# Optimization experiments

Hardware: AMD Instinct MI355X
Metric: run time of the kernel (lower is better)

## Reference

```python
import jax, jax.numpy as jnp
import numpy as np

L, H, D, E, V, MAXS = 12, 12, 64, 768, 50257, 1024

def _ln(x, g, b, eps=1e-5):
    m = jnp.mean(x, axis=-1, keepdims=True)
    v = jnp.mean(jnp.square(x - m), axis=-1, keepdims=True)
    return (x - m) * jax.lax.rsqrt(v + eps) * g + b

def setup_inputs() -> dict:
    key = jax.random.key(0)
    ks = jax.random.split(key, 16)
    s = 0.02
    inp = {
        "input_ids": jax.random.randint(ks[0], (1, 1), 0, V),
        "past_key": jax.random.normal(ks[1], (L, 1, H, MAXS, D), jnp.float32),
        "past_value": jax.random.normal(ks[2], (L, 1, H, MAXS, D), jnp.float32),
        "past_seq_len": 1023,
        "attention_mask": jnp.ones((1, MAXS), jnp.float32),
        "wte": jax.random.normal(ks[3], (V, E), jnp.float32) * s,
        "wpe": jax.random.normal(ks[4], (MAXS, E), jnp.float32) * s,
        "ln1_g": jnp.ones((L, E), jnp.float32),
        "ln1_b": jnp.zeros((L, E), jnp.float32),
        "attn_w": jax.random.normal(ks[5], (L, E, 3 * E), jnp.float32) * s,
        "attn_b": jnp.zeros((L, 3 * E), jnp.float32),
        "proj_w": jax.random.normal(ks[6], (L, E, E), jnp.float32) * s,
        "proj_b": jnp.zeros((L, E), jnp.float32),
        "ln2_g": jnp.ones((L, E), jnp.float32),
        "ln2_b": jnp.zeros((L, E), jnp.float32),
        "fc_w": jax.random.normal(ks[7], (L, E, 4 * E), jnp.float32) * s,
        "fc_b": jnp.zeros((L, 4 * E), jnp.float32),
        "mlp_w": jax.random.normal(ks[8], (L, 4 * E, E), jnp.float32) * s,
        "mlp_b": jnp.zeros((L, E), jnp.float32),
        "lnf_g": jnp.ones((E,), jnp.float32),
        "lnf_b": jnp.zeros((E,), jnp.float32),
    }
    return inp

def reference(input_ids, past_key, past_value, past_seq_len, attention_mask,
              wte, wpe, ln1_g, ln1_b, attn_w, attn_b, proj_w, proj_b,
              ln2_g, ln2_b, fc_w, fc_b, mlp_w, mlp_b, lnf_g, lnf_b):
    S = int(past_seq_len)  # static cache length
    h = wte[input_ids] + wpe[S]                      # [1,1,E]
    bias = (1.0 - attention_mask[:, :S + 1]) * -1e9  # [1,S+1]
    scale = 1.0 / jnp.sqrt(jnp.float32(D))
    pk, pv = past_key, past_value
    for l in range(L):
        x = _ln(h, ln1_g[l], ln1_b[l])
        qkv = x @ attn_w[l] + attn_b[l]              # [1,1,3E]
        q, k, v = jnp.split(qkv, 3, axis=-1)
        q = q.reshape(1, 1, H, D).transpose(0, 2, 1, 3)  # [1,H,1,D]
        k = k.reshape(1, 1, H, D).transpose(0, 2, 1, 3)
        v = v.reshape(1, 1, H, D).transpose(0, 2, 1, 3)
        k_full = jnp.concatenate([pk[l, :, :, :S, :], k], axis=2)  # [1,H,S+1,D]
        v_full = jnp.concatenate([pv[l, :, :, :S, :], v], axis=2)
        scores = jnp.einsum('bhqd,bhkd->bhqk', q, k_full) * scale
        scores = scores + bias[:, None, None, :]
        attn = jax.nn.softmax(scores, axis=-1)
        o = jnp.einsum('bhqk,bhkd->bhqd', attn, v_full)
        o = o.transpose(0, 2, 1, 3).reshape(1, 1, H * D)
        h = h + o @ proj_w[l] + proj_b[l]
        x2 = _ln(h, ln2_g[l], ln2_b[l])
        h = h + jax.nn.gelu(x2 @ fc_w[l] + fc_b[l], approximate=True) @ mlp_w[l] + mlp_b[l]
        pk = pk.at[l, :, :, S, :].set(k[:, :, 0, :])
        pv = pv.at[l, :, :, S, :].set(v[:, :, 0, :])
    h = _ln(h, lnf_g, lnf_b)
    logits = h @ wte.T                               # [1,1,V] (tied lm_head)
    return (logits, pk, pv)
```

## Files before the change

### kernel.cpp

```cpp
#include <hip/hip_runtime.h>
#include <math.h>

#define EMB 768
#define NH 12
#define HD 64
#define NL 12
#define NV 50257
#define MAXS 1024
#define S_PAST 1023
#define E3 2304
#define E4 3072

#define WS_H    0
#define WS_QKV  768
#define WS_FC   3072
#define WS_PART 6144

__device__ __forceinline__ void blockReduce2(float& a, float& b, volatile float* ra, volatile float* rb) {
  int lane = threadIdx.x & 63, wid = threadIdx.x >> 6;
#pragma unroll
  for (int o = 32; o > 0; o >>= 1) { a += __shfl_down(a, o); b += __shfl_down(b, o); }
  if (lane == 0) { ra[wid] = a; rb[wid] = b; }
  __syncthreads();
  if (threadIdx.x == 0) {
    ra[0] = ra[0] + ra[1] + ra[2] + ra[3];
    rb[0] = rb[0] + rb[1] + rb[2] + rb[3];
  }
  __syncthreads();
  a = ra[0]; b = rb[0];
}

__global__ void init_kernel(const int* __restrict__ ids, const float* __restrict__ wte,
                            const float* __restrict__ wpe, const float* __restrict__ attn_b,
                            float* __restrict__ hvec, float* __restrict__ qkv) {
  int idx = blockIdx.x * 256 + threadIdx.x;
  if (idx < E3) qkv[idx] = attn_b[idx];
  if (idx < EMB) {
    int id = ids[0];
    hvec[idx] = wte[(size_t)id * EMB + idx] + wpe[(size_t)S_PAST * EMB + idx];
  }
}

__global__ void ln_gemv4(const float* __restrict__ hvec, const float* __restrict__ g,
                         const float* __restrict__ bb, const float* __restrict__ W,
                         float* __restrict__ out, int N, int l) {
  __shared__ float lh[EMB];
  __shared__ float xs[32];
  __shared__ float ra[4], rb[4];
  __shared__ float4 red[4][64];
  int tid = threadIdx.x, lane = tid & 63, wid = tid >> 6;
  int e0 = blockIdx.y * 32;
  float hv0 = hvec[tid], hv1 = hvec[tid + 256], hv2 = hvec[tid + 512];
  int j4 = blockIdx.x * 64 + lane;
  int N4 = N >> 2;
  const float4* p = (const float4*)(W + (size_t)l * EMB * N) + (size_t)(e0 + wid) * N4 + j4;
  float4 w[8];
#pragma unroll
  for (int i = 0; i < 8; i++) w[i] = p[(size_t)(i * 4) * N4];
  float gv = 0.f, bv = 0.f;
  if (tid < 32) { gv = g[l * EMB + e0 + tid]; bv = bb[l * EMB + e0 + tid]; }
  lh[tid] = hv0; lh[tid + 256] = hv1; lh[tid + 512] = hv2;
  float s1 = hv0 + hv1 + hv2;
  float s2 = hv0 * hv0 + hv1 * hv1 + hv2 * hv2;
  blockReduce2(s1, s2, ra, rb);
  float mean = s1 * (1.f / EMB);
  float var = s2 * (1.f / EMB) - mean * mean;
  float rstd = rsqrtf(var + 1e-5f);
  if (tid < 32) xs[tid] = (lh[e0 + tid] - mean) * rstd * gv + bv;
  __syncthreads();
  float4 acc = {0.f, 0.f, 0.f, 0.f};
#pragma unroll
  for (int i = 0; i < 8; i++) {
    float x = xs[wid + i * 4];
    acc.x += x * w[i].x; acc.y += x * w[i].y; acc.z += x * w[i].z; acc.w += x * w[i].w;
  }
  red[wid][lane] = acc;
  __syncthreads();
  if (wid == 0) {
    float4 a0 = red[0][lane], a1 = red[1][lane], a2 = red[2][lane], a3 = red[3][lane];
    float rx = a0.x + a1.x + a2.x + a3.x;
    float ry = a0.y + a1.y + a2.y + a3.y;
    float rz = a0.z + a1.z + a2.z + a3.z;
    float rw = a0.w + a1.w + a2.w + a3.w;
    float* op = out + (size_t)j4 * 4;
    atomicAdd(op + 0, rx); atomicAdd(op + 1, ry);
    atomicAdd(op + 2, rz); atomicAdd(op + 3, rw);
  }
}

__global__ void attn_kv(const float* __restrict__ qkv, const float* __restrict__ pk,
                        const float* __restrict__ pv, const float* __restrict__ mask,
                        float* __restrict__ opk, float* __restrict__ opv,
                        float* __restrict__ part, int l) {
  int h = blockIdx.x >> 4, c = blockIdx.x & 15;
  int tid = threadIdx.x, lane = tid & 63, wid = tid >> 6;
  int sub = tid & 15, grp = tid >> 4;
  __shared__ float4 qs4[16];
  __shared__ float sc[64];
  __shared__ float4 redo[4][16];
  if (tid < 16) qs4[tid] = ((const float4*)(qkv + h * 64))[tid];
  __syncthreads();
  size_t base = ((size_t)(l * NH + h) * MAXS) * HD;
  const float4* K4 = (const float4*)(pk + base);
  const float4* V4 = (const float4*)(pv + base);
  float4* oK4 = (float4*)(opk + base);
  float4* oV4 = (float4*)(opv + base);
  int t0 = c * 64;
  float4 kreg[4];
#pragma unroll
  for (int i = 0; i < 4; i++) {
    int t = t0 + grp + i * 16;
    kreg[i] = (t == S_PAST) ? ((const float4*)(qkv + EMB + h * 64))[sub] : K4[(size_t)t * 16 + sub];
  }
#pragma unroll
  for (int i = 0; i < 4; i++) {
    int t = t0 + grp + i * 16;
    oK4[(size_t)t * 16 + sub] = kreg[i];
  }
  float4 q4 = qs4[sub];
#pragma unroll
  for (int i = 0; i < 4; i++) {
    int key = grp + i * 16;
    float p = q4.x * kreg[i].x + q4.y * kreg[i].y + q4.z * kreg[i].z + q4.w * kreg[i].w;
    p += __shfl_xor(p, 1); p += __shfl_xor(p, 2);
    p += __shfl_xor(p, 4); p += __shfl_xor(p, 8);
    if (sub == 0) sc[key] = p * 0.125f + (1.f - mask[t0 + key]) * (-1e9f);
  }
  __syncthreads();
  if (wid == 0) {
    float a = sc[lane];
    float m = a;
#pragma unroll
    for (int o = 32; o > 0; o >>= 1) m = fmaxf(m, __shfl_down(m, o));
    m = __shfl(m, 0);
    float ea = expf(a - m);
    sc[lane] = ea;
    float s = ea;
#pragma unroll
    for (int o = 32; o > 0; o >>= 1) s += __shfl_down(s, o);
    if (lane == 0) { part[(h * 16 + c) * 68 + 0] = m; part[(h * 16 + c) * 68 + 1] = s; }
  }
  __syncthreads();
  float4 vreg[4];
#pragma unroll
  for (int i = 0; i < 4; i++) {
    int t = t0 + grp + i * 16;
    vreg[i] = (t == S_PAST) ? ((const float4*)(qkv + 2 * EMB + h * 64))[sub] : V4[(size_t)t * 16 + sub];
  }
#pragma unroll
  for (int i = 0; i < 4; i++) {
    int t = t0 + grp + i * 16;
    oV4[(size_t)t * 16 + sub] = vreg[i];
  }
  float4 acc = {0.f, 0.f, 0.f, 0.f};
#pragma unroll
  for (int i = 0; i < 4; i++) {
    float w = sc[grp + i * 16];
    acc.x += w * vreg[i].x; acc.y += w * vreg[i].y; acc.z += w * vreg[i].z; acc.w += w * vreg[i].w;
  }
  acc.x += __shfl_xor(acc.x, 16); acc.y += __shfl_xor(acc.y, 16);
  acc.z += __shfl_xor(acc.z, 16); acc.w += __shfl_xor(acc.w, 16);
  acc.x += __shfl_xor(acc.x, 32); acc.y += __shfl_xor(acc.y, 32);
  acc.z += __shfl_xor(acc.z, 32); acc.w += __shfl_xor(acc.w, 32);
  if (lane < 16) redo[wid][lane] = acc;
  __syncthreads();
  if (tid < 16) {
    float4 a0 = redo[0][tid], a1 = redo[1][tid], a2 = redo[2][tid], a3 = redo[3][tid];
    float4 r;
    r.x = a0.x + a1.x + a2.x + a3.x;
    r.y = a0.y + a1.y + a2.y + a3.y;
    r.z = a0.z + a1.z + a2.z + a3.z;
    r.w = a0.w + a1.w + a2.w + a3.w;
    ((float4*)(part + (h * 16 + c) * 68 + 4))[tid] = r;
  }
}

__global__ void proj_attn(const float* __restrict__ part, const float* __restrict__ W,
                          const float* __restrict__ bias, const float* __restrict__ fc_b,
                          float* __restrict__ hout, float* __restrict__ wfc, int l) {
  int jb = blockIdx.x;
  int rt = blockIdx.y;
  int h = rt >> 2, esub = rt & 3;
  int tid = threadIdx.x, lane = tid & 63, wid = tid >> 6;
  __shared__ float xs[16];
  __shared__ float4 red[4][64];
  int j4 = jb * 64 + lane;
  const int N4 = EMB >> 2;
  int r0 = h * 64 + esub * 16;
  const float4* p = (const float4*)(W + (size_t)l * EMB * EMB) + (size_t)(r0 + wid) * N4 + j4;
  float4 w[4];
#pragma unroll
  for (int i = 0; i < 4; i++) w[i] = p[(size_t)(i * 4) * N4];
  if (tid < 16) {
    float M = -1e30f;
#pragma unroll
    for (int q = 0; q < 16; q++) M = fmaxf(M, part[(h * 16 + q) * 68]);
    float T = 0.f, o = 0.f;
    int d = esub * 16 + tid;
#pragma unroll
    for (int q = 0; q < 16; q++) {
      float wq = expf(part[(h * 16 + q) * 68] - M);
      T += part[(h * 16 + q) * 68 + 1] * wq;
      o += part[(h * 16 + q) * 68 + 4 + d] * wq;
    }
    xs[tid] = o / T;
  }
  int bid = rt * 3 + jb;
  if (bid < 12) wfc[bid * 256 + tid] = fc_b[l * E4 + bid * 256 + tid];
  __syncthreads();
  float4 acc = {0.f, 0.f, 0.f, 0.f};
#pragma unroll
  for (int i = 0; i < 4; i++) {
    float x = xs[wid + i * 4];
    acc.x += x * w[i].x; acc.y += x * w[i].y; acc.z += x * w[i].z; acc.w += x * w[i].w;
  }
  red[wid][lane] = acc;
  __syncthreads();
  if (wid == 0) {
    float4 a0 = red[0][lane], a1 = red[1][lane], a2 = red[2][lane], a3 = red[3][lane];
    float rx = a0.x + a1.x + a2.x + a3.x;
    float ry = a0.y + a1.y + a2.y + a3.y;
    float rz = a0.z + a1.z + a2.z + a3.z;
    float rw = a0.w + a1.w + a2.w + a3.w;
    if (rt == 0) {
      const float* bp = bias + l * EMB + jb * 256 + lane * 4;
      rx += bp[0]; ry += bp[1]; rz += bp[2]; rw += bp[3];
    }
    float* op = hout + (size_t)jb * 256 + (size_t)lane * 4;
    atomicAdd(op + 0, rx); atomicAdd(op + 1, ry);
    atomicAdd(op + 2, rz); atomicAdd(op + 3, rw);
  }
}

__global__ void mlp_gemv4(const float* __restrict__ fcv, const float* __restrict__ W,
                          const float* __restrict__ bias, const float* __restrict__ attn_b,
                          float* __restrict__ hout, float* __restrict__ qkv, int l) {
  __shared__ float xs[64];
  __shared__ float4 red[4][64];
  int tid = threadIdx.x, lane = tid & 63, wid = tid >> 6;
  int e0 = blockIdx.y * 64;
  int j4 = blockIdx.x * 64 + lane;
  const int N4 = EMB >> 2;
  const float4* p = (const float4*)(W + (size_t)l * E4 * EMB) + (size_t)(e0 + wid) * N4 + j4;
  float4 w[16];
#pragma unroll
  for (int i = 0; i < 16; i++) w[i] = p[(size_t)(i * 4) * N4];
  if (tid < 64) {
    float x = fcv[e0 + tid];
    xs[tid] = 0.5f * x * (1.f + tanhf(0.7978845608028654f * (x + 0.044715f * x * x * x)));
  }
  int bid = blockIdx.y * 3 + blockIdx.x;
  if (l + 1 < NL && bid < 9) qkv[bid * 256 + tid] = attn_b[(l + 1) * E3 + bid * 256 + tid];
  __syncthreads();
  float4 acc = {0.f, 0.f, 0.f, 0.f};
#pragma unroll
  for (int i = 0; i < 16; i++) {
    float x = xs[wid + i * 4];
    acc.x += x * w[i].x; acc.y += x * w[i].y; acc.z += x * w[i].z; acc.w += x * w[i].w;
  }
  red[wid][lane] = acc;
  __syncthreads();
  if (wid == 0) {
    float4 a0 = red[0][lane], a1 = red[1][lane], a2 = red[2][lane], a3 = red[3][lane];
    float rx = a0.x + a1.x + a2.x + a3.x;
    float ry = a0.y + a1.y + a2.y + a3.y;
    float rz = a0.z + a1.z + a2.z + a3.z;
    float rw = a0.w + a1.w + a2.w + a3.w;
    if (blockIdx.y == 0) {
      const float* bp = bias + l * EMB + j4 * 4;
      rx += bp[0]; ry += bp[1]; rz += bp[2]; rw += bp[3];
    }
    float* op = hout + (size_t)j4 * 4;
    atomicAdd(op + 0, rx); atomicAdd(op + 1, ry);
    atomicAdd(op + 2, rz); atomicAdd(op + 3, rw);
  }
}

__global__ void logits_lnf(const float* __restrict__ hvec, const float* __restrict__ g,
                           const float* __restrict__ b, const float* __restrict__ wte,
                           float* __restrict__ out) {
  __shared__ float4 xs4[192];
  __shared__ float ra[4], rb[4];
  int tid = threadIdx.x, lane = tid & 63, wid = tid >> 6;
  float hv0 = hvec[tid], hv1 = hvec[tid + 256], hv2 = hvec[tid + 512];
  int v = blockIdx.x * 4 + wid;
  float4 a0 = {0,0,0,0}, a1 = {0,0,0,0}, a2 = {0,0,0,0};
  if (v < NV) {
    const float4* row = (const float4*)(wte + (size_t)v * EMB);
    a0 = row[lane]; a1 = row[lane + 64]; a2 = row[lane + 128];
  }
  float s1 = hv0 + hv1 + hv2;
  float s2 = hv0 * hv0 + hv1 * hv1 + hv2 * hv2;
  blockReduce2(s1, s2, ra, rb);
  float mean = s1 * (1.f / EMB);
  float var = s2 * (1.f / EMB) - mean * mean;
  float rstd = rsqrtf(var + 1e-5f);
  ((float*)xs4)[tid]       = (hv0 - mean) * rstd * g[tid]       + b[tid];
  ((float*)xs4)[tid + 256] = (hv1 - mean) * rstd * g[tid + 256] + b[tid + 256];
  ((float*)xs4)[tid + 512] = (hv2 - mean) * rstd * g[tid + 512] + b[tid + 512];
  __syncthreads();
  if (v >= NV) return;
  float4 x0 = xs4[lane], x1 = xs4[lane + 64], x2 = xs4[lane + 128];
  float acc = a0.x * x0.x + a0.y * x0.y + a0.z * x0.z + a0.w * x0.w
            + a1.x * x1.x + a1.y * x1.y + a1.z * x1.z + a1.w * x1.w
            + a2.x * x2.x + a2.y * x2.y + a2.z * x2.z + a2.w * x2.w;
#pragma unroll
  for (int o = 32; o > 0; o >>= 1) acc += __shfl_down(acc, o);
  if (lane == 0) out[v] = acc;
}

extern "C" void kernel_launch(void* const* d_in, const int* in_sizes, int n_in,
                              void* d_out, int out_size, void* d_ws, size_t ws_size,
                              hipStream_t stream) {
  const int* input_ids = (const int*)d_in[0];
  const float* past_key = (const float*)d_in[1];
  const float* past_value = (const float*)d_in[2];
  const float* mask = (const float*)d_in[4];
  const float* wte = (const float*)d_in[5];
  const float* wpe = (const float*)d_in[6];
  const float* ln1_g = (const float*)d_in[7];
  const float* ln1_b = (const float*)d_in[8];
  const float* attn_w = (const float*)d_in[9];
  const float* attn_b = (const float*)d_in[10];
  const float* proj_w = (const float*)d_in[11];
  const float* proj_b = (const float*)d_in[12];
  const float* ln2_g = (const float*)d_in[13];
  const float* ln2_b = (const float*)d_in[14];
  const float* fc_w = (const float*)d_in[15];
  const float* fc_b = (const float*)d_in[16];
  const float* mlp_w = (const float*)d_in[17];
  const float* mlp_b = (const float*)d_in[18];
  const float* lnf_g = (const float*)d_in[19];
  const float* lnf_b = (const float*)d_in[20];

  float* out = (float*)d_out;
  float* out_logits = out;
  float* out_pk = out + NV;
  float* out_pv = out_pk + (size_t)NL * NH * MAXS * HD;

  float* ws = (float*)d_ws;
  float* wh = ws + WS_H;
  float* wqkv = ws + WS_QKV;
  float* wfc = ws + WS_FC;
  float* wpart = ws + WS_PART;

  init_kernel<<<9, 256, 0, stream>>>(input_ids, wte, wpe, attn_b, wh, wqkv);

  for (int l = 0; l < NL; l++) {
    ln_gemv4<<<dim3(9, 24), 256, 0, stream>>>(wh, ln1_g, ln1_b, attn_w, wqkv, E3, l);
    attn_kv<<<192, 256, 0, stream>>>(wqkv, past_key, past_value, mask, out_pk, out_pv, wpart, l);
    proj_attn<<<dim3(3, 48), 256, 0, stream>>>(wpart, proj_w, proj_b, fc_b, wh, wfc, l);
    ln_gemv4<<<dim3(12, 24), 256, 0, stream>>>(wh, ln2_g, ln2_b, fc_w, wfc, E4, l);
    mlp_gemv4<<<dim3(3, 48), 256, 0, stream>>>(wfc, mlp_w, mlp_b, attn_b, wh, wqkv, l);
  }
  logits_lnf<<<12565, 256, 0, stream>>>(wh, lnf_g, lnf_b, wte, out_logits);
}
```

Baseline: 448.5 us.

## Fuse LN1 and QKV projection into attention kernel, handle new token separately

```diff
diff --git a/kernel.cpp b/kernel.cpp
--- a/kernel.cpp
+++ b/kernel.cpp
@@ -12,9 +12,17 @@
 #define E4 3072
 
 #define WS_H    0
-#define WS_QKV  768
-#define WS_FC   3072
-#define WS_PART 6144
+#define WS_FC   768
+#define WS_PART 3840
+#define WS_VNEW 16896
+#define WS_DOT  17088
+
+__device__ __forceinline__ void f4add(float4& a, const float4& b) {
+  a.x += b.x; a.y += b.y; a.z += b.z; a.w += b.w;
+}
+__device__ __forceinline__ void f4fma(float4& a, float x, const float4& w) {
+  a.x += x * w.x; a.y += x * w.y; a.z += x * w.z; a.w += x * w.w;
+}
 
 __device__ __forceinline__ void blockReduce2(float& a, float& b, volatile float* ra, volatile float* rb) {
   int lane = threadIdx.x & 63, wid = threadIdx.x >> 6;
@@ -30,103 +38,152 @@
   a = ra[0]; b = rb[0];
 }
 
+__device__ __forceinline__ float gelu(float x) {
+  return 0.5f * x * (1.f + tanhf(0.7978845608028654f * (x + 0.044715f * x * x * x)));
+}
+
 __global__ void init_kernel(const int* __restrict__ ids, const float* __restrict__ wte,
-                            const float* __restrict__ wpe, const float* __restrict__ attn_b,
-                            float* __restrict__ hvec, float* __restrict__ qkv) {
-  int idx = blockIdx.x * 256 + threadIdx.x;
-  if (idx < E3) qkv[idx] = attn_b[idx];
-  if (idx < EMB) {
-    int id = ids[0];
-    hvec[idx] = wte[(size_t)id * EMB + idx] + wpe[(size_t)S_PAST * EMB + idx];
-  }
-}
-
-__global__ void ln_gemv4(const float* __restrict__ hvec, const float* __restrict__ g,
-                         const float* __restrict__ bb, const float* __restrict__ W,
-                         float* __restrict__ out, int N, int l) {
-  __shared__ float lh[EMB];
-  __shared__ float xs[32];
-  __shared__ float ra[4], rb[4];
-  __shared__ float4 red[4][64];
+                            const float* __restrict__ wpe, float* __restrict__ wsf) {
+  int tid = threadIdx.x;
+  int id = ids[0];
+#pragma unroll
+  for (int k = 0; k < 3; k++) {
+    int e = tid + 256 * k;
+    wsf[WS_H + e] = wte[(size_t)id * EMB + e] + wpe[(size_t)S_PAST * EMB + e];
+  }
+  if (tid < NL * NH) wsf[WS_DOT + tid] = 0.f;
+}
+
+__global__ void attn_fused(const float* __restrict__ pk, const float* __restrict__ pv,
+                           const float* __restrict__ mask,
+                           const float* __restrict__ ln1_g, const float* __restrict__ ln1_b,
+                           const float* __restrict__ attn_w, const float* __restrict__ attn_b,
+                           float* __restrict__ opk, float* __restrict__ opv,
+                           float* __restrict__ wsf, int l) {
+  __shared__ __align__(16) float smem[1936];
+  float* xs = smem;
+  volatile float* ra = smem + 768;
+  volatile float* rb = smem + 772;
+  float4* qls = (float4*)(smem + 776);
+  float* sc = smem + 848;
+  float4* red = (float4*)(smem + 912);
+  int bi = blockIdx.x;
+  int h = bi % NH, c = bi / NH;
   int tid = threadIdx.x, lane = tid & 63, wid = tid >> 6;
-  int e0 = blockIdx.y * 32;
-  float hv0 = hvec[tid], hv1 = hvec[tid + 256], hv2 = hvec[tid + 512];
-  int j4 = blockIdx.x * 64 + lane;
-  int N4 = N >> 2;
-  const float4* p = (const float4*)(W + (size_t)l * EMB * N) + (size_t)(e0 + wid) * N4 + j4;
-  float4 w[8];
-#pragma unroll
-  for (int i = 0; i < 8; i++) w[i] = p[(size_t)(i * 4) * N4];
-  float gv = 0.f, bv = 0.f;
-  if (tid < 32) { gv = g[l * EMB + e0 + tid]; bv = bb[l * EMB + e0 + tid]; }
-  lh[tid] = hv0; lh[tid + 256] = hv1; lh[tid + 512] = hv2;
-  float s1 = hv0 + hv1 + hv2;
-  float s2 = hv0 * hv0 + hv1 * hv1 + hv2 * hv2;
+  int sub = tid & 15, grp = tid >> 4;
+  const float* wh = wsf + WS_H;
+  float hv0 = wh[tid], hv1 = wh[tid + 256], hv2 = wh[tid + 512];
+  size_t base = ((size_t)(l * NH + h) * MAXS) * HD;
+  const float4* K4 = (const float4*)(pk + base);
+  const float4* V4 = (const float4*)(pv + base);
+  int t0 = c * 64;
+  float4 kreg[4];
+#pragma unroll
+  for (int i = 0; i < 4; i++) {
+    int t = t0 + grp + i * 16;
+    kreg[i] = K4[(size_t)t * 16 + sub];
+  }
+  float gv0 = ln1_g[l * EMB + tid], gv1 = ln1_g[l * EMB + tid + 256], gv2 = ln1_g[l * EMB + tid + 512];
+  float bv0 = ln1_b[l * EMB + tid], bv1 = ln1_b[l * EMB + tid + 256], bv2 = ln1_b[l * EMB + tid + 512];
+  float s1 = hv0 + hv1 + hv2, s2 = hv0 * hv0 + hv1 * hv1 + hv2 * hv2;
   blockReduce2(s1, s2, ra, rb);
   float mean = s1 * (1.f / EMB);
   float var = s2 * (1.f / EMB) - mean * mean;
   float rstd = rsqrtf(var + 1e-5f);
-  if (tid < 32) xs[tid] = (lh[e0 + tid] - mean) * rstd * gv + bv;
-  __syncthreads();
-  float4 acc = {0.f, 0.f, 0.f, 0.f};
-#pragma unroll
-  for (int i = 0; i < 8; i++) {
-    float x = xs[wid + i * 4];
-    acc.x += x * w[i].x; acc.y += x * w[i].y; acc.z += x * w[i].z; acc.w += x * w[i].w;
-  }
-  red[wid][lane] = acc;
-  __syncthreads();
-  if (wid == 0) {
-    float4 a0 = red[0][lane], a1 = red[1][lane], a2 = red[2][lane], a3 = red[3][lane];
-    float rx = a0.x + a1.x + a2.x + a3.x;
-    float ry = a0.y + a1.y + a2.y + a3.y;
-    float rz = a0.z + a1.z + a2.z + a3.z;
-    float rw = a0.w + a1.w + a2.w + a3.w;
-    float* op = out + (size_t)j4 * 4;
-    atomicAdd(op + 0, rx); atomicAdd(op + 1, ry);
-    atomicAdd(op + 2, rz); atomicAdd(op + 3, rw);
-  }
-}
-
-__global__ void attn_kv(const float* __restrict__ qkv, const float* __restrict__ pk,
-                        const float* __restrict__ pv, const float* __restrict__ mask,
-                        float* __restrict__ opk, float* __restrict__ opv,
-                        float* __restrict__ part, int l) {
-  int h = blockIdx.x >> 4, c = blockIdx.x & 15;
-  int tid = threadIdx.x, lane = tid & 63, wid = tid >> 6;
-  int sub = tid & 15, grp = tid >> 4;
-  __shared__ float4 qs4[16];
-  __shared__ float sc[64];
-  __shared__ float4 redo[4][16];
-  if (tid < 16) qs4[tid] = ((const float4*)(qkv + h * 64))[tid];
-  __syncthreads();
-  size_t base = ((size_t)(l * NH + h) * MAXS) * HD;
-  const float4* K4 = (const float4*)(pk + base);
-  const float4* V4 = (const float4*)(pv + base);
-  float4* oK4 = (float4*)(opk + base);
-  float4* oV4 = (float4*)(opv + base);
-  int t0 = c * 64;
-  float4 kreg[4];
-#pragma unroll
-  for (int i = 0; i < 4; i++) {
-    int t = t0 + grp + i * 16;
-    kreg[i] = (t == S_PAST) ? ((const float4*)(qkv + EMB + h * 64))[sub] : K4[(size_t)t * 16 + sub];
-  }
-#pragma unroll
-  for (int i = 0; i < 4; i++) {
-    int t = t0 + grp + i * 16;
-    oK4[(size_t)t * 16 + sub] = kreg[i];
-  }
-  float4 q4 = qs4[sub];
+  xs[tid]       = (hv0 - mean) * rstd * gv0 + bv0;
+  xs[tid + 256] = (hv1 - mean) * rstd * gv1 + bv1;
+  xs[tid + 512] = (hv2 - mean) * rstd * gv2 + bv2;
+  __syncthreads();
+  const float4* Wb4 = (const float4*)(attn_w + (size_t)l * EMB * E3);
+  const int STR = E3 >> 2;
+  const float4* Wq4 = Wb4 + h * 16 + sub;
+  float4 qacc = {0.f, 0.f, 0.f, 0.f};
+#pragma unroll
+  for (int b = 0; b < 4; b++) {
+    float4 w[12];
+#pragma unroll
+    for (int j = 0; j < 12; j++) w[j] = Wq4[(size_t)(grp + 16 * (b * 12 + j)) * STR];
+#pragma unroll
+    for (int j = 0; j < 12; j++) f4fma(qacc, xs[grp + 16 * (b * 12 + j)], w[j]);
+  }
+  red[tid] = qacc;
+  __syncthreads();
+#pragma unroll
+  for (int s = 8; s >= 1; s >>= 1) {
+    if (tid < s * 16) f4add(red[tid], red[tid + s * 16]);
+    __syncthreads();
+  }
+  if (tid < 16) {
+    float4 q = red[tid];
+    f4add(q, ((const float4*)(attn_b + l * E3 + h * 64))[tid]);
+    qls[tid] = q;
+  }
+  __syncthreads();
+  const float4* Wk4 = Wb4 + 192 + h * 16 + c;
+  const float4* Wv4 = Wb4 + 384 + h * 16 + c;
+  float4 ak = {0.f, 0.f, 0.f, 0.f}, av = {0.f, 0.f, 0.f, 0.f};
+  {
+    float4 wk[3], wv[3];
+#pragma unroll
+    for (int j = 0; j < 3; j++) {
+      int r = tid + 256 * j;
+      wk[j] = Wk4[(size_t)r * STR]; wv[j] = Wv4[(size_t)r * STR];
+    }
+#pragma unroll
+    for (int j = 0; j < 3; j++) {
+      int r = tid + 256 * j;
+      f4fma(ak, xs[r], wk[j]); f4fma(av, xs[r], wv[j]);
+    }
+  }
+  red[tid] = ak;
+  __syncthreads();
+#pragma unroll
+  for (int s = 128; s >= 1; s >>= 1) {
+    if (tid < s) f4add(red[tid], red[tid + s]);
+    __syncthreads();
+  }
+  if (tid == 0) {
+    float4 kn = red[0];
+    f4add(kn, ((const float4*)(attn_b + l * E3))[192 + h * 16 + c]);
+    qls[16] = kn;
+  }
+  __syncthreads();
+  red[tid] = av;
+  __syncthreads();
+#pragma unroll
+  for (int s = 128; s >= 1; s >>= 1) {
+    if (tid < s) f4add(red[tid], red[tid + s]);
+    __syncthreads();
+  }
+  if (tid == 0) {
+    float4 vn = red[0];
+    f4add(vn, ((const float4*)(attn_b + l * E3))[384 + h * 16 + c]);
+    float4 kn = qls[16];
+    const float* qf = (const float*)qls;
+    float d4 = qf[c * 4] * kn.x + qf[c * 4 + 1] * kn.y + qf[c * 4 + 2] * kn.z + qf[c * 4 + 3] * kn.w;
+    atomicAdd(wsf + WS_DOT + l * NH + h, d4);
+    ((float4*)(opk + base))[(size_t)S_PAST * 16 + c] = kn;
+    ((float4*)(opv + base))[(size_t)S_PAST * 16 + c] = vn;
+    ((float4*)(wsf + WS_VNEW))[h * 16 + c] = vn;
+  }
+  float4 q4 = qls[sub];
 #pragma unroll
   for (int i = 0; i < 4; i++) {
     int key = grp + i * 16;
+    int t = t0 + key;
     float p = q4.x * kreg[i].x + q4.y * kreg[i].y + q4.z * kreg[i].z + q4.w * kreg[i].w;
     p += __shfl_xor(p, 1); p += __shfl_xor(p, 2);
     p += __shfl_xor(p, 4); p += __shfl_xor(p, 8);
-    if (sub == 0) sc[key] = p * 0.125f + (1.f - mask[t0 + key]) * (-1e9f);
-  }
-  __syncthreads();
+    if (sub == 0) sc[key] = (t == S_PAST) ? -1e9f : p * 0.125f + (1.f - mask[t]) * (-1e9f);
+  }
+  float4 vreg[4];
+#pragma unroll
+  for (int i = 0; i < 4; i++) {
+    int t = t0 + grp + i * 16;
+    vreg[i] = V4[(size_t)t * 16 + sub];
+  }
+  __syncthreads();
+  float* part = wsf + WS_PART;
   if (wid == 0) {
     float a = sc[lane];
     float m = a;
@@ -141,31 +198,20 @@
     if (lane == 0) { part[(h * 16 + c) * 68 + 0] = m; part[(h * 16 + c) * 68 + 1] = s; }
   }
   __syncthreads();
-  float4 vreg[4];
-#pragma unroll
-  for (int i = 0; i < 4; i++) {
-    int t = t0 + grp + i * 16;
-    vreg[i] = (t == S_PAST) ? ((const float4*)(qkv + 2 * EMB + h * 64))[sub] : V4[(size_t)t * 16 + sub];
-  }
-#pragma unroll
-  for (int i = 0; i < 4; i++) {
-    int t = t0 + grp + i * 16;
-    oV4[(size_t)t * 16 + sub] = vreg[i];
-  }
   float4 acc = {0.f, 0.f, 0.f, 0.f};
 #pragma unroll
   for (int i = 0; i < 4; i++) {
     float w = sc[grp + i * 16];
-    acc.x += w * vreg[i].x; acc.y += w * vreg[i].y; acc.z += w * vreg[i].z; acc.w += w * vreg[i].w;
+    f4fma(acc, w, vreg[i]);
   }
   acc.x += __shfl_xor(acc.x, 16); acc.y += __shfl_xor(acc.y, 16);
   acc.z += __shfl_xor(acc.z, 16); acc.w += __shfl_xor(acc.w, 16);
   acc.x += __shfl_xor(acc.x, 32); acc.y += __shfl_xor(acc.y, 32);
   acc.z += __shfl_xor(acc.z, 32); acc.w += __shfl_xor(acc.w, 32);
-  if (lane < 16) redo[wid][lane] = acc;
+  if (lane < 16) red[wid * 16 + lane] = acc;
   __syncthreads();
   if (tid < 16) {
-    float4 a0 = redo[0][tid], a1 = redo[1][tid], a2 = redo[2][tid], a3 = redo[3][tid];
+    float4 a0 = red[tid], a1 = red[16 + tid], a2 = red[32 + tid], a3 = red[48 + tid];
     float4 r;
     r.x = a0.x + a1.x + a2.x + a3.x;
     r.y = a0.y + a1.y + a2.y + a3.y;
@@ -173,17 +219,27 @@
     r.w = a0.w + a1.w + a2.w + a3.w;
     ((float4*)(part + (h * 16 + c) * 68 + 4))[tid] = r;
   }
-}
-
-__global__ void proj_attn(const float* __restrict__ part, const float* __restrict__ W,
-                          const float* __restrict__ bias, const float* __restrict__ fc_b,
-                          float* __restrict__ hout, float* __restrict__ wfc, int l) {
+#pragma unroll
+  for (int i = 0; i < 4; i++) {
+    int t = t0 + grp + i * 16;
+    if (t != S_PAST) {
+      ((float4*)(opk + base))[(size_t)t * 16 + sub] = kreg[i];
+      ((float4*)(opv + base))[(size_t)t * 16 + sub] = vreg[i];
+    }
+  }
+}
+
+__global__ void proj_attn(const float* __restrict__ W, const float* __restrict__ bias,
+                          const float* __restrict__ fc_b, const float* __restrict__ mask,
+                          float* __restrict__ hout, float* __restrict__ wsf, int l) {
   int jb = blockIdx.x;
   int rt = blockIdx.y;
   int h = rt >> 2, esub = rt & 3;
   int tid = threadIdx.x, lane = tid & 63, wid = tid >> 6;
   __shared__ float xs[16];
   __shared__ float4 red[4][64];
+  const float* part = wsf + WS_PART;
+  float* wfc = wsf + WS_FC;
   int j4 = jb * 64 + lane;
   const int N4 = EMB >> 2;
   int r0 = h * 64 + esub * 16;
@@ -192,11 +248,13 @@
 #pragma unroll
   for (int i = 0; i < 4; i++) w[i] = p[(size_t)(i * 4) * N4];
   if (tid < 16) {
-    float M = -1e30f;
+    float dot8 = wsf[WS_DOT + l * NH + h] * 0.125f + (1.f - mask[S_PAST]) * (-1e9f);
+    float M = dot8;
 #pragma unroll
     for (int q = 0; q < 16; q++) M = fmaxf(M, part[(h * 16 + q) * 68]);
-    float T = 0.f, o = 0.f;
+    float en = expf(dot8 - M);
     int d = esub * 16 + tid;
+    float T = en, o = en * wsf[WS_VNEW + h * 64 + d];
 #pragma unroll
     for (int q = 0; q < 16; q++) {
       float wq = expf(part[(h * 16 + q) * 68] - M);
@@ -210,10 +268,7 @@
   __syncthreads();
   float4 acc = {0.f, 0.f, 0.f, 0.f};
 #pragma unroll
-  for (int i = 0; i < 4; i++) {
-    float x = xs[wid + i * 4];
-    acc.x += x * w[i].x; acc.y += x * w[i].y; acc.z += x * w[i].z; acc.w += x * w[i].w;
-  }
+  for (int i = 0; i < 4; i++) f4fma(acc, xs[wid + i * 4], w[i]);
   red[wid][lane] = acc;
   __syncthreads();
   if (wid == 0) {
@@ -232,9 +287,52 @@
   }
 }
 
+__global__ void fc_gemv(const float* __restrict__ hvec, const float* __restrict__ g,
+                        const float* __restrict__ bb, const float* __restrict__ W,
+                        float* __restrict__ wfc, int l) {
+  __shared__ float lh[EMB];
+  __shared__ float xs[48];
+  __shared__ float ra[4], rb[4];
+  __shared__ float4 red[4][64];
+  int tid = threadIdx.x, lane = tid & 63, wid = tid >> 6;
+  int jt = blockIdx.x, et = blockIdx.y;
+  int e0 = et * 48;
+  float hv0 = hvec[tid], hv1 = hvec[tid + 256], hv2 = hvec[tid + 512];
+  int j4 = jt * 64 + lane;
+  const int N4 = E4 >> 2;
+  const float4* p = (const float4*)(W + (size_t)l * EMB * E4) + (size_t)(e0 + wid) * N4 + j4;
+  float4 w[12];
+#pragma unroll
+  for (int i = 0; i < 12; i++) w[i] = p[(size_t)(i * 4) * N4];
+  float gv = 0.f, bv = 0.f;
+  if (tid < 48) { gv = g[l * EMB + e0 + tid]; bv = bb[l * EMB + e0 + tid]; }
+  lh[tid] = hv0; lh[tid + 256] = hv1; lh[tid + 512] = hv2;
+  float s1 = hv0 + hv1 + hv2, s2 = hv0 * hv0 + hv1 * hv1 + hv2 * hv2;
+  blockReduce2(s1, s2, ra, rb);
+  float mean = s1 * (1.f / EMB);
+  float var = s2 * (1.f / EMB) - mean * mean;
+  float rstd = rsqrtf(var + 1e-5f);
+  if (tid < 48) xs[tid] = (lh[e0 + tid] - mean) * rstd * gv + bv;
+  __syncthreads();
+  float4 acc = {0.f, 0.f, 0.f, 0.f};
+#pragma unroll
+  for (int i = 0; i < 12; i++) f4fma(acc, xs[wid + i * 4], w[i]);
+  red[wid][lane] = acc;
+  __syncthreads();
+  if (wid == 0) {
+    float4 a0 = red[0][lane], a1 = red[1][lane], a2 = red[2][lane], a3 = red[3][lane];
+    float rx = a0.x + a1.x + a2.x + a3.x;
+    float ry = a0.y + a1.y + a2.y + a3.y;
+    float rz = a0.z + a1.z + a2.z + a3.z;
+    float rw = a0.w + a1.w + a2.w + a3.w;
+    float* op = wfc + (size_t)j4 * 4;
+    atomicAdd(op + 0, rx); atomicAdd(op + 1, ry);
+    atomicAdd(op + 2, rz); atomicAdd(op + 3, rw);
+  }
+}
+
 __global__ void mlp_gemv4(const float* __restrict__ fcv, const float* __restrict__ W,
-                          const float* __restrict__ bias, const float* __restrict__ attn_b,
-                          float* __restrict__ hout, float* __restrict__ qkv, int l) {
+                          const float* __restrict__ bias, float* __restrict__ hout, int l) {
   __shared__ float xs[64];
   __shared__ float4 red[4][64];
   int tid = threadIdx.x, lane = tid & 63, wid = tid >> 6;
@@ -245,19 +343,11 @@
   float4 w[16];
 #pragma unroll
   for (int i = 0; i < 16; i++) w[i] = p[(size_t)(i * 4) * N4];
-  if (tid < 64) {
-    float x = fcv[e0 + tid];
-    xs[tid] = 0.5f * x * (1.f + tanhf(0.7978845608028654f * (x + 0.044715f * x * x * x)));
-  }
-  int bid = blockIdx.y * 3 + blockIdx.x;
-  if (l + 1 < NL && bid < 9) qkv[bid * 256 + tid] = attn_b[(l + 1) * E3 + bid * 256 + tid];
+  if (tid < 64) xs[tid] = gelu(fcv[e0 + tid]);
   __syncthreads();
   float4 acc = {0.f, 0.f, 0.f, 0.f};
 #pragma unroll
-  for (int i = 0; i < 16; i++) {
-    float x = xs[wid + i * 4];
-    acc.x += x * w[i].x; acc.y += x * w[i].y; acc.z += x * w[i].z; acc.w += x * w[i].w;
-  }
+  for (int i = 0; i < 16; i++) f4fma(acc, xs[wid + i * 4], w[i]);
   red[wid][lane] = acc;
   __syncthreads();
   if (wid == 0) {
@@ -279,7 +369,7 @@
 __global__ void logits_lnf(const float* __restrict__ hvec, const float* __restrict__ g,
                            const float* __restrict__ b, const float* __restrict__ wte,
                            float* __restrict__ out) {
-  __shared__ float4 xs4[192];
+  __shared__ __align__(16) float4 xs4[192];
   __shared__ float ra[4], rb[4];
   int tid = threadIdx.x, lane = tid & 63, wid = tid >> 6;
   float hv0 = hvec[tid], hv1 = hvec[tid + 256], hv2 = hvec[tid + 512];
@@ -337,21 +427,18 @@
   float* out_logits = out;
   float* out_pk = out + NV;
   float* out_pv = out_pk + (size_t)NL * NH * MAXS * HD;
-
-  float* ws = (float*)d_ws;
-  float* wh = ws + WS_H;
-  float* wqkv = ws + WS_QKV;
-  float* wfc = ws + WS_FC;
-  float* wpart = ws + WS_PART;
-
-  init_kernel<<<9, 256, 0, stream>>>(input_ids, wte, wpe, attn_b, wh, wqkv);
+  float* wsf = (float*)d_ws;
+  float* wh = wsf + WS_H;
+  float* wfc = wsf + WS_FC;
+
+  init_kernel<<<1, 256, 0, stream>>>(input_ids, wte, wpe, wsf);
 
   for (int l = 0; l < NL; l++) {
-    ln_gemv4<<<dim3(9, 24), 256, 0, stream>>>(wh, ln1_g, ln1_b, attn_w, wqkv, E3, l);
-    attn_kv<<<192, 256, 0, stream>>>(wqkv, past_key, past_value, mask, out_pk, out_pv, wpart, l);
-    proj_attn<<<dim3(3, 48), 256, 0, stream>>>(wpart, proj_w, proj_b, fc_b, wh, wfc, l);
-    ln_gemv4<<<dim3(12, 24), 256, 0, stream>>>(wh, ln2_g, ln2_b, fc_w, wfc, E4, l);
-    mlp_gemv4<<<dim3(3, 48), 256, 0, stream>>>(wfc, mlp_w, mlp_b, attn_b, wh, wqkv, l);
+    attn_fused<<<192, 256, 0, stream>>>(past_key, past_value, mask, ln1_g, ln1_b,
+                                        attn_w, attn_b, out_pk, out_pv, wsf, l);
+    proj_attn<<<dim3(3, 48), 256, 0, stream>>>(proj_w, proj_b, fc_b, mask, wh, wsf, l);
+    fc_gemv<<<dim3(12, 16), 256, 0, stream>>>(wh, ln2_g, ln2_b, fc_w, wfc, l);
+    mlp_gemv4<<<dim3(3, 48), 256, 0, stream>>>(wfc, mlp_w, mlp_b, wh, l);
   }
   logits_lnf<<<12565, 256, 0, stream>>>(wh, lnf_g, lnf_b, wte, out_logits);
 }
```

Result: slower. 500.5 us (+11.6%).

## Fuse FC and MLP GEMVs into one kernel with double-buffered hidden state

Applied to the files above, without the earlier changes.

```diff
diff --git a/kernel.cpp b/kernel.cpp
--- a/kernel.cpp
+++ b/kernel.cpp
@@ -11,10 +11,17 @@
 #define E3 2304
 #define E4 3072
 
-#define WS_H    0
-#define WS_QKV  768
-#define WS_FC   3072
-#define WS_PART 6144
+#define WS_HA   0
+#define WS_HB   768
+#define WS_QKV  1536
+#define WS_PART 3840
+
+__device__ __forceinline__ void f4add(float4& a, const float4& b) {
+  a.x += b.x; a.y += b.y; a.z += b.z; a.w += b.w;
+}
+__device__ __forceinline__ void f4fma(float4& a, float x, const float4& w) {
+  a.x += x * w.x; a.y += x * w.y; a.z += x * w.z; a.w += x * w.w;
+}
 
 __device__ __forceinline__ void blockReduce2(float& a, float& b, volatile float* ra, volatile float* rb) {
   int lane = threadIdx.x & 63, wid = threadIdx.x >> 6;
@@ -30,20 +37,24 @@
   a = ra[0]; b = rb[0];
 }
 
+__device__ __forceinline__ float gelu(float x) {
+  return 0.5f * x * (1.f + tanhf(0.7978845608028654f * (x + 0.044715f * x * x * x)));
+}
+
 __global__ void init_kernel(const int* __restrict__ ids, const float* __restrict__ wte,
                             const float* __restrict__ wpe, const float* __restrict__ attn_b,
-                            float* __restrict__ hvec, float* __restrict__ qkv) {
+                            float* __restrict__ wsf) {
   int idx = blockIdx.x * 256 + threadIdx.x;
-  if (idx < E3) qkv[idx] = attn_b[idx];
+  if (idx < E3) wsf[WS_QKV + idx] = attn_b[idx];
   if (idx < EMB) {
     int id = ids[0];
-    hvec[idx] = wte[(size_t)id * EMB + idx] + wpe[(size_t)S_PAST * EMB + idx];
-  }
-}
-
-__global__ void ln_gemv4(const float* __restrict__ hvec, const float* __restrict__ g,
-                         const float* __restrict__ bb, const float* __restrict__ W,
-                         float* __restrict__ out, int N, int l) {
+    wsf[WS_HA + idx] = wte[(size_t)id * EMB + idx] + wpe[(size_t)S_PAST * EMB + idx];
+  }
+}
+
+__global__ void ln_gemv4(const float* __restrict__ hvec, float* __restrict__ shadow,
+                         const float* __restrict__ g, const float* __restrict__ bb,
+                         const float* __restrict__ W, float* __restrict__ out, int l) {
   __shared__ float lh[EMB];
   __shared__ float xs[32];
   __shared__ float ra[4], rb[4];
@@ -52,13 +63,16 @@
   int e0 = blockIdx.y * 32;
   float hv0 = hvec[tid], hv1 = hvec[tid + 256], hv2 = hvec[tid + 512];
   int j4 = blockIdx.x * 64 + lane;
-  int N4 = N >> 2;
-  const float4* p = (const float4*)(W + (size_t)l * EMB * N) + (size_t)(e0 + wid) * N4 + j4;
+  const int N4 = E3 >> 2;
+  const float4* p = (const float4*)(W + (size_t)l * EMB * E3) + (size_t)(e0 + wid) * N4 + j4;
   float4 w[8];
 #pragma unroll
   for (int i = 0; i < 8; i++) w[i] = p[(size_t)(i * 4) * N4];
   float gv = 0.f, bv = 0.f;
   if (tid < 32) { gv = g[l * EMB + e0 + tid]; bv = bb[l * EMB + e0 + tid]; }
+  if (blockIdx.x == 0 && blockIdx.y == 0) {
+    shadow[tid] = hv0; shadow[tid + 256] = hv1; shadow[tid + 512] = hv2;
+  }
   lh[tid] = hv0; lh[tid + 256] = hv1; lh[tid + 512] = hv2;
   float s1 = hv0 + hv1 + hv2;
   float s2 = hv0 * hv0 + hv1 * hv1 + hv2 * hv2;
@@ -70,10 +84,7 @@
   __syncthreads();
   float4 acc = {0.f, 0.f, 0.f, 0.f};
 #pragma unroll
-  for (int i = 0; i < 8; i++) {
-    float x = xs[wid + i * 4];
-    acc.x += x * w[i].x; acc.y += x * w[i].y; acc.z += x * w[i].z; acc.w += x * w[i].w;
-  }
+  for (int i = 0; i < 8; i++) f4fma(acc, xs[wid + i * 4], w[i]);
   red[wid][lane] = acc;
   __syncthreads();
   if (wid == 0) {
@@ -154,10 +165,7 @@
   }
   float4 acc = {0.f, 0.f, 0.f, 0.f};
 #pragma unroll
-  for (int i = 0; i < 4; i++) {
-    float w = sc[grp + i * 16];
-    acc.x += w * vreg[i].x; acc.y += w * vreg[i].y; acc.z += w * vreg[i].z; acc.w += w * vreg[i].w;
-  }
+  for (int i = 0; i < 4; i++) f4fma(acc, sc[grp + i * 16], vreg[i]);
   acc.x += __shfl_xor(acc.x, 16); acc.y += __shfl_xor(acc.y, 16);
   acc.z += __shfl_xor(acc.z, 16); acc.w += __shfl_xor(acc.w, 16);
   acc.x += __shfl_xor(acc.x, 32); acc.y += __shfl_xor(acc.y, 32);
@@ -176,8 +184,8 @@
 }
 
 __global__ void proj_attn(const float* __restrict__ part, const float* __restrict__ W,
-                          const float* __restrict__ bias, const float* __restrict__ fc_b,
-                          float* __restrict__ hout, float* __restrict__ wfc, int l) {
+                          const float* __restrict__ bias, float* __restrict__ houtR,
+                          float* __restrict__ houtS, int l) {
   int jb = blockIdx.x;
   int rt = blockIdx.y;
   int h = rt >> 2, esub = rt & 3;
@@ -205,15 +213,10 @@
     }
     xs[tid] = o / T;
   }
-  int bid = rt * 3 + jb;
-  if (bid < 12) wfc[bid * 256 + tid] = fc_b[l * E4 + bid * 256 + tid];
   __syncthreads();
   float4 acc = {0.f, 0.f, 0.f, 0.f};
 #pragma unroll
-  for (int i = 0; i < 4; i++) {
-    float x = xs[wid + i * 4];
-    acc.x += x * w[i].x; acc.y += x * w[i].y; acc.z += x * w[i].z; acc.w += x * w[i].w;
-  }
+  for (int i = 0; i < 4; i++) f4fma(acc, xs[wid + i * 4], w[i]);
   red[wid][lane] = acc;
   __syncthreads();
   if (wid == 0) {
@@ -226,60 +229,96 @@
       const float* bp = bias + l * EMB + jb * 256 + lane * 4;
       rx += bp[0]; ry += bp[1]; rz += bp[2]; rw += bp[3];
     }
-    float* op = hout + (size_t)jb * 256 + (size_t)lane * 4;
-    atomicAdd(op + 0, rx); atomicAdd(op + 1, ry);
-    atomicAdd(op + 2, rz); atomicAdd(op + 3, rw);
-  }
-}
-
-__global__ void mlp_gemv4(const float* __restrict__ fcv, const float* __restrict__ W,
-                          const float* __restrict__ bias, const float* __restrict__ attn_b,
-                          float* __restrict__ hout, float* __restrict__ qkv, int l) {
-  __shared__ float xs[64];
-  __shared__ float4 red[4][64];
-  int tid = threadIdx.x, lane = tid & 63, wid = tid >> 6;
-  int e0 = blockIdx.y * 64;
-  int j4 = blockIdx.x * 64 + lane;
-  const int N4 = EMB >> 2;
-  const float4* p = (const float4*)(W + (size_t)l * E4 * EMB) + (size_t)(e0 + wid) * N4 + j4;
-  float4 w[16];
-#pragma unroll
-  for (int i = 0; i < 16; i++) w[i] = p[(size_t)(i * 4) * N4];
-  if (tid < 64) {
-    float x = fcv[e0 + tid];
-    xs[tid] = 0.5f * x * (1.f + tanhf(0.7978845608028654f * (x + 0.044715f * x * x * x)));
-  }
-  int bid = blockIdx.y * 3 + blockIdx.x;
-  if (l + 1 < NL && bid < 9) qkv[bid * 256 + tid] = attn_b[(l + 1) * E3 + bid * 256 + tid];
+    size_t off = (size_t)jb * 256 + (size_t)lane * 4;
+    float* op1 = houtR + off;
+    atomicAdd(op1 + 0, rx); atomicAdd(op1 + 1, ry);
+    atomicAdd(op1 + 2, rz); atomicAdd(op1 + 3, rw);
+    float* op2 = houtS + off;
+    atomicAdd(op2 + 0, rx); atomicAdd(op2 + 1, ry);
+    atomicAdd(op2 + 2, rz); atomicAdd(op2 + 3, rw);
+  }
+}
+
+__global__ __launch_bounds__(256) void fcmlp(
+    const float* __restrict__ hvec, float* __restrict__ hshadow,
+    const float* __restrict__ g2, const float* __restrict__ b2,
+    const float* __restrict__ fc_w, const float* __restrict__ fc_b,
+    const float* __restrict__ mlp_w, const float* __restrict__ mlp_b,
+    const float* __restrict__ attn_b, float* __restrict__ wqkv, int l) {
+  __shared__ float xs[EMB];
+  __shared__ float ra[4], rb[4];
+  __shared__ __align__(16) float4 red[256];
+  __shared__ float gl[16];
+  __shared__ __align__(16) float4 arr[768];
+  int tid = threadIdx.x, lane = tid & 63, wid = tid >> 6;
+  int bi = blockIdx.x;
+  float hv0 = hvec[tid], hv1 = hvec[tid + 256], hv2 = hvec[tid + 512];
+  int q = tid & 3, r0 = tid >> 2;
+  const float4* WA = (const float4*)(fc_w + (size_t)l * EMB * E4) + (size_t)bi * 4 + q;
+  float4 wa[12];
+#pragma unroll
+  for (int i = 0; i < 12; i++) wa[i] = WA[(size_t)(r0 + 64 * i) * (E4 >> 2)];
+  const float4* WB = (const float4*)(mlp_w + (size_t)l * E4 * EMB) + (size_t)(bi * 16 + wid * 4) * (EMB >> 2) + lane;
+  float4 wb[12];
+#pragma unroll
+  for (int i = 0; i < 4; i++)
+#pragma unroll
+    for (int k = 0; k < 3; k++) wb[i * 3 + k] = WB[(size_t)i * (EMB >> 2) + 64 * k];
+  float gv0 = g2[l * EMB + tid], gv1 = g2[l * EMB + tid + 256], gv2 = g2[l * EMB + tid + 512];
+  float bv0 = b2[l * EMB + tid], bv1 = b2[l * EMB + tid + 256], bv2 = b2[l * EMB + tid + 512];
+  if (l + 1 < NL && bi < 9) wqkv[bi * 256 + tid] = attn_b[(l + 1) * E3 + bi * 256 + tid];
+  float s1 = hv0 + hv1 + hv2, s2 = hv0 * hv0 + hv1 * hv1 + hv2 * hv2;
+  blockReduce2(s1, s2, ra, rb);
+  float mean = s1 * (1.f / EMB);
+  float var = s2 * (1.f / EMB) - mean * mean;
+  float rstd = rsqrtf(var + 1e-5f);
+  xs[tid]       = (hv0 - mean) * rstd * gv0 + bv0;
+  xs[tid + 256] = (hv1 - mean) * rstd * gv1 + bv1;
+  xs[tid + 512] = (hv2 - mean) * rstd * gv2 + bv2;
   __syncthreads();
   float4 acc = {0.f, 0.f, 0.f, 0.f};
 #pragma unroll
-  for (int i = 0; i < 16; i++) {
-    float x = xs[wid + i * 4];
-    acc.x += x * w[i].x; acc.y += x * w[i].y; acc.z += x * w[i].z; acc.w += x * w[i].w;
-  }
-  red[wid][lane] = acc;
+  for (int i = 0; i < 12; i++) f4fma(acc, xs[r0 + 64 * i], wa[i]);
+  red[tid] = acc;
+  __syncthreads();
+#pragma unroll
+  for (int s = 128; s >= 4; s >>= 1) {
+    if (tid < s) f4add(red[tid], red[tid + s]);
+    __syncthreads();
+  }
+  if (tid < 16) gl[tid] = gelu(((const float*)red)[tid] + fc_b[l * E4 + bi * 16 + tid]);
+  __syncthreads();
+  float4 a0 = {0.f,0.f,0.f,0.f}, a1 = {0.f,0.f,0.f,0.f}, a2 = {0.f,0.f,0.f,0.f};
+#pragma unroll
+  for (int i = 0; i < 4; i++) {
+    float x = gl[wid * 4 + i];
+    f4fma(a0, x, wb[i * 3]); f4fma(a1, x, wb[i * 3 + 1]); f4fma(a2, x, wb[i * 3 + 2]);
+  }
+  arr[wid * 192 + lane] = a0;
+  arr[wid * 192 + lane + 64] = a1;
+  arr[wid * 192 + lane + 128] = a2;
   __syncthreads();
   if (wid == 0) {
-    float4 a0 = red[0][lane], a1 = red[1][lane], a2 = red[2][lane], a3 = red[3][lane];
-    float rx = a0.x + a1.x + a2.x + a3.x;
-    float ry = a0.y + a1.y + a2.y + a3.y;
-    float rz = a0.z + a1.z + a2.z + a3.z;
-    float rw = a0.w + a1.w + a2.w + a3.w;
-    if (blockIdx.y == 0) {
-      const float* bp = bias + l * EMB + j4 * 4;
-      rx += bp[0]; ry += bp[1]; rz += bp[2]; rw += bp[3];
+#pragma unroll
+    for (int k = 0; k < 3; k++) {
+      int cf = lane + 64 * k;
+      float4 v = arr[cf];
+      f4add(v, arr[192 + cf]); f4add(v, arr[384 + cf]); f4add(v, arr[576 + cf]);
+      if (bi == 0) {
+        const float* bp = mlp_b + l * EMB + cf * 4;
+        v.x += bp[0]; v.y += bp[1]; v.z += bp[2]; v.w += bp[3];
+      }
+      float* op = hshadow + (size_t)cf * 4;
+      atomicAdd(op + 0, v.x); atomicAdd(op + 1, v.y);
+      atomicAdd(op + 2, v.z); atomicAdd(op + 3, v.w);
     }
-    float* op = hout + (size_t)j4 * 4;
-    atomicAdd(op + 0, rx); atomicAdd(op + 1, ry);
-    atomicAdd(op + 2, rz); atomicAdd(op + 3, rw);
   }
 }
 
 __global__ void logits_lnf(const float* __restrict__ hvec, const float* __restrict__ g,
                            const float* __restrict__ b, const float* __restrict__ wte,
                            float* __restrict__ out) {
-  __shared__ float4 xs4[192];
+  __shared__ __align__(16) float4 xs4[192];
   __shared__ float ra[4], rb[4];
   int tid = threadIdx.x, lane = tid & 63, wid = tid >> 6;
   float hv0 = hvec[tid], hv1 = hvec[tid + 256], hv2 = hvec[tid + 512];
@@ -338,20 +377,20 @@
   float* out_pk = out + NV;
   float* out_pv = out_pk + (size_t)NL * NH * MAXS * HD;
 
-  float* ws = (float*)d_ws;
-  float* wh = ws + WS_H;
-  float* wqkv = ws + WS_QKV;
-  float* wfc = ws + WS_FC;
-  float* wpart = ws + WS_PART;
-
-  init_kernel<<<9, 256, 0, stream>>>(input_ids, wte, wpe, attn_b, wh, wqkv);
+  float* wsf = (float*)d_ws;
+  float* wqkv = wsf + WS_QKV;
+  float* wpart = wsf + WS_PART;
+
+  init_kernel<<<9, 256, 0, stream>>>(input_ids, wte, wpe, attn_b, wsf);
 
   for (int l = 0; l < NL; l++) {
-    ln_gemv4<<<dim3(9, 24), 256, 0, stream>>>(wh, ln1_g, ln1_b, attn_w, wqkv, E3, l);
+    float* R = wsf + ((l & 1) ? WS_HB : WS_HA);
+    float* S = wsf + ((l & 1) ? WS_HA : WS_HB);
+    ln_gemv4<<<dim3(9, 24), 256, 0, stream>>>(R, S, ln1_g, ln1_b, attn_w, wqkv, l);
     attn_kv<<<192, 256, 0, stream>>>(wqkv, past_key, past_value, mask, out_pk, out_pv, wpart, l);
-    proj_attn<<<dim3(3, 48), 256, 0, stream>>>(wpart, proj_w, proj_b, fc_b, wh, wfc, l);
-    ln_gemv4<<<dim3(12, 24), 256, 0, stream>>>(wh, ln2_g, ln2_b, fc_w, wfc, E4, l);
-    mlp_gemv4<<<dim3(3, 48), 256, 0, stream>>>(wfc, mlp_w, mlp_b, attn_b, wh, wqkv, l);
-  }
-  logits_lnf<<<12565, 256, 0, stream>>>(wh, lnf_g, lnf_b, wte, out_logits);
-}
+    proj_attn<<<dim3(3, 48), 256, 0, stream>>>(wpart, proj_w, proj_b, R, S, l);
+    fcmlp<<<192, 256, 0, stream>>>(R, S, ln2_g, ln2_b, fc_w, fc_b, mlp_w, mlp_b,
+                                   attn_b, wqkv, l);
+  }
+  logits_lnf<<<12565, 256, 0, stream>>>(wsf + WS_HA, lnf_g, lnf_b, wte, out_logits);
+}
```

New measurement: 581.9 us. +29.7%, slower.
